# Optimization experiments

Measured on AMD Instinct MI355X. Metric: run time of the kernel, lower is better.

Reference implementation:

```python
import jax, jax.numpy as jnp
import numpy as np

H = 1024   # LSTM hidden (hardcoded in init_states)
A = 128    # attention / speaker dim
M = 80     # mel channels
TXT = 512  # text embedding dim
E = TXT + A
V = 185    # Flowtron symbol vocab
T = 512    # mel frames
TT = 192   # text tokens
SCALE = 0.05


def setup_inputs() -> dict:
    key = jax.random.key(0)
    ks = jax.random.split(key, 24)
    def rn(k, shape, s=SCALE):
        return jax.random.normal(k, shape, jnp.float32) * s
    return {
        "residual": jax.random.normal(ks[0], (1, M, T), jnp.float32),
        "speaker_vecs": jax.random.normal(ks[1], (1, A), jnp.float32),
        "emb": rn(ks[2], (V, TXT), 1.0),
        "Wih_att": rn(ks[3], (2, 4 * H, M)),
        "Whh_att": rn(ks[4], (2, 4 * H, H)),
        "b_att": jnp.zeros((2, 4 * H), jnp.float32),
        "Wq": rn(ks[5], (2, H, A)),
        "Wk": rn(ks[6], (2, E, A)),
        "Wv": rn(ks[7], (2, E, A)),
        "Wih1": rn(ks[8], (2, 4 * H, H + A)),
        "Whh1": rn(ks[9], (2, 4 * H, H)),
        "b1": jnp.zeros((2, 4 * H), jnp.float32),
        "Wih2": rn(ks[10], (2, 4 * H, H)),
        "Whh2": rn(ks[11], (2, 4 * H, H)),
        "b2": jnp.zeros((2, 4 * H), jnp.float32),
        "Wd": rn(ks[12], (2, H, H)),
        "bd": jnp.zeros((2, H), jnp.float32),
        "Wo": rn(ks[13], (2, H, 2 * M), 0.01),
        "bo": jnp.zeros((2, 2 * M), jnp.float32),
        "Wg": rn(ks[14], (2, H + A, 1)),
        "bg": jnp.zeros((2, 1), jnp.float32),
        "text": jax.random.randint(ks[15], (1, TT), 0, V),
    }


def _cell(x, h, c, Wih, Whh, b):
    # standard LSTM cell, gate order i,f,g,o
    z = x @ Wih.T + h @ Whh.T + b
    i, f, g, o = jnp.split(z, 4, axis=-1)
    c = jax.nn.sigmoid(f) * c + jax.nn.sigmoid(i) * jnp.tanh(g)
    h = jax.nn.sigmoid(o) * jnp.tanh(c)
    return h, c


def _run_flow(seq, enc, p, reverse):
    (Wih_att, Whh_att, b_att, Wq, Wk, Wv, Wih1, Whh1, b1,
     Wih2, Whh2, b2, Wd, bd, Wo, bo, Wg, bg) = p
    keys = enc @ Wk   # [TT, A] precomputed outside the scan
    vals = enc @ Wv   # [TT, A]
    inv = jnp.float32(1.0 / np.sqrt(A))
    def step(carry, x_t):
        prev, ha, ca, h1, c1, h2, c2 = carry
        ha, ca = _cell(prev, ha, ca, Wih_att, Whh_att, b_att)
        attn = jax.nn.softmax((ha @ Wq) @ keys.T * inv, axis=-1)  # [1, TT]
        ctx = attn @ vals                                          # [1, A]
        di = jnp.concatenate([ha, ctx], axis=-1)                   # [1, H+A]
        gate = jax.nn.sigmoid(di @ Wg + bg)  # gate computed; early-exit replaced by full-length scan
        h1, c1 = _cell(di, h1, c1, Wih1, Whh1, b1)
        h2, c2 = _cell(h1, h2, c2, Wih2, Whh2, b2)
        hd = jnp.tanh(h2 @ Wd + bd)
        out = hd @ Wo + bo
        b_p, log_s = jnp.split(out, 2, axis=-1)
        y = (x_t - b_p) * jnp.exp(-log_s)   # inverse affine coupling
        return (y, ha, ca, h1, c1, h2, c2), y
    z0 = jnp.zeros((1, M), seq.dtype)
    zh = jnp.zeros((1, H), seq.dtype)
    xs = seq[::-1] if reverse else seq
    _, ys = jax.lax.scan(step, (z0, zh, zh, zh, zh, zh, zh), xs)  # ys: [T, 1, M]
    return ys[::-1] if reverse else ys


def reference(residual, speaker_vecs, emb, Wih_att, Whh_att, b_att, Wq, Wk, Wv,
              Wih1, Whh1, b1, Wih2, Whh2, b2, Wd, bd, Wo, bo, Wg, bg, text):
    # encoder: text embedding concat broadcast speaker vector -> [TT, E]
    enc = jnp.concatenate(
        [emb[text[0]], jnp.broadcast_to(speaker_vecs, (text.shape[1], speaker_vecs.shape[1]))], axis=-1)
    stacked = (Wih_att, Whh_att, b_att, Wq, Wk, Wv, Wih1, Whh1, b1,
               Wih2, Whh2, b2, Wd, bd, Wo, bo, Wg, bg)
    seq = jnp.transpose(residual, (2, 0, 1))   # [T, 1, M]
    seq = _run_flow(seq, enc, tuple(w[1] for w in stacked), reverse=True)   # backward flow
    seq = _run_flow(seq, enc, tuple(w[0] for w in stacked), reverse=False)  # forward flow
    return jnp.transpose(seq, (1, 2, 0))       # [1, M, T]
```

## Files before the change

kernel.cpp:

```cpp
#include <hip/hip_runtime.h>
#include <hip/hip_bf16.h>
#include <stdint.h>

#define AG __HIP_MEMORY_SCOPE_AGENT
typedef unsigned long long ull;

static constexpr size_t OFF_WA  = 0;
static constexpr size_t OFF_W1  = 18874368;
static constexpr size_t OFF_W2  = 54657024;
static constexpr size_t OFF_WD  = 88342528;
static constexpr size_t OFF_WO  = 92536832;
static constexpr size_t OFF_WQ  = 93192192;
static constexpr size_t OFF_VL  = 93978624;
static constexpr size_t OFF_KEY = 94109696;
static constexpr size_t OFF_V32 = 94306304;
static constexpr size_t OFF_WQT = 94502912;
static constexpr size_t OFF_ENC = 95551488;
static constexpr size_t OFF_RB  = 96043008;
static constexpr size_t OFF_SEQ = 96206848;
static constexpr size_t OFF_DYN = 96370688;
static constexpr size_t OFF_HAb = OFF_DYN + 0;
static constexpr size_t OFF_H1b = OFF_DYN + 4096;
static constexpr size_t OFF_H2b = OFF_DYN + 8192;
static constexpr size_t OFF_HDb = OFF_DYN + 12288;
static constexpr size_t OFF_YBb = OFF_DYN + 16384;
static constexpr size_t OFF_SCb = OFF_DYN + 16896;
static constexpr size_t OFF_CXb = OFF_DYN + 17920;
static constexpr size_t OFF_FLG = OFF_DYN + 18432;
static constexpr size_t DYN_BYTES = 18432 + 229376;
static constexpr size_t NEEDED = OFF_DYN + DYN_BYTES;

#define PA 0
#define PS 1
#define P1 2
#define P2 3
#define PD 4
#define PF 5

__device__ __forceinline__ float aldx(const float* p){ return __hip_atomic_load(p, __ATOMIC_RELAXED, AG); }
__device__ __forceinline__ void  astx(float* p, float v){ __hip_atomic_store(p, v, __ATOMIC_RELAXED, AG); }
__device__ __forceinline__ ull   aldx8(const ull* p){ return __hip_atomic_load(p, __ATOMIC_RELAXED, AG); }
__device__ __forceinline__ int   ldi(const int* p){ return __hip_atomic_load(p, __ATOMIC_RELAXED, AG); }
__device__ __forceinline__ int   PADI(int k){ return k + ((k>>5)<<2); }

__device__ __forceinline__ float dot8(uint4 w, const float* v){
  float4 a = *(const float4*)v;
  float4 b = *(const float4*)(v+4);
  float s;
  s = __uint_as_float(w.x << 16) * a.x;
  s = fmaf(__uint_as_float(w.x & 0xffff0000u), a.y, s);
  s = fmaf(__uint_as_float(w.y << 16),         a.z, s);
  s = fmaf(__uint_as_float(w.y & 0xffff0000u), a.w, s);
  s = fmaf(__uint_as_float(w.z << 16),         b.x, s);
  s = fmaf(__uint_as_float(w.z & 0xffff0000u), b.y, s);
  s = fmaf(__uint_as_float(w.w << 16),         b.z, s);
  s = fmaf(__uint_as_float(w.w & 0xffff0000u), b.w, s);
  return s;
}
__device__ __forceinline__ float dot4(uint2 w, const float* v){
  float4 a = *(const float4*)v;
  float s;
  s = __uint_as_float(w.x << 16) * a.x;
  s = fmaf(__uint_as_float(w.x & 0xffff0000u), a.y, s);
  s = fmaf(__uint_as_float(w.y << 16),         a.z, s);
  s = fmaf(__uint_as_float(w.y & 0xffff0000u), a.w, s);
  return s;
}
__device__ __forceinline__ float sigf(float x){ return 1.f/(1.f+__expf(-x)); }
__device__ __forceinline__ float tanhf_(float x){
  x = fminf(12.f, fmaxf(-12.f, x));
  float t = __expf(2.f*x);
  return (t-1.f)/(t+1.f);
}

__global__ void k_init(float* z, int n){ int i = blockIdx.x*256 + threadIdx.x; if (i<n) z[i]=0.f; }

__global__ void k_rbuf(const float* res, float* rb){
  int i = blockIdx.x*256 + threadIdx.x; if (i >= 512*80) return;
  int t = i/80, m = i - t*80;
  rb[i] = res[m*512 + t];
}

__global__ void k_enc(const float* emb, const float* spk, const int* text, float* enc){
  int i = blockIdx.x*256 + threadIdx.x; if (i >= 192*640) return;
  int s = i/640, e = i - s*640;
  enc[i] = (e < 512) ? emb[(size_t)text[s]*512 + e] : spk[e-512];
}

__global__ void k_keysvals(const float* enc, const float* Wk, const float* Wv,
                           float* keys, float* vals32){
  int i = blockIdx.x*256 + threadIdx.x; if (i >= 2*192*128) return;
  int f = i/(192*128); int r = i - f*192*128; int s = r/128, a = r - s*128;
  float ka=0.f, va=0.f;
  for (int e=0;e<640;++e){
    float x = enc[s*640+e];
    ka = fmaf(x, Wk[((size_t)f*640+e)*128+a], ka);
    va = fmaf(x, Wv[((size_t)f*640+e)*128+a], va);
  }
  keys[((size_t)f*192+s)*128+a] = ka;
  vals32[((size_t)f*192+s)*128+a] = va;
}

__global__ void k_wqT(const float* Wq, float* WqT){
  int i = blockIdx.x*256 + threadIdx.x; if (i >= 2*128*1024) return;
  int f = i/(128*1024); int r = i - f*128*1024; int a = r/1024, h = r - a*1024;
  WqT[i] = Wq[((size_t)f*1024+h)*128+a];
}

__global__ void k_wqk2(const float* WqT, const float* keys, uint2* dst){
  int b = blockIdx.x; int f = b/192, s = b - f*192;
  int t = threadIdx.x;
  float4 acc = {0.f,0.f,0.f,0.f};
  const float* kp = keys + ((size_t)f*192+s)*128;
  const float* wp = WqT + (size_t)f*128*1024 + t*4;
  for (int a=0;a<128;++a){
    float kk = kp[a];
    float4 w = *(const float4*)(wp + (size_t)a*1024);
    acc.x = fmaf(kk, w.x, acc.x); acc.y = fmaf(kk, w.y, acc.y);
    acc.z = fmaf(kk, w.z, acc.z); acc.w = fmaf(kk, w.w, acc.w);
  }
  const float inv = 0.08838834764831845f;
  __hip_bfloat16 b0 = __float2bfloat16(acc.x*inv), b1 = __float2bfloat16(acc.y*inv);
  __hip_bfloat16 b2 = __float2bfloat16(acc.z*inv), b3 = __float2bfloat16(acc.w*inv);
  uint2 o;
  o.x = (uint32_t)(*(uint16_t*)&b0) | ((uint32_t)(*(uint16_t*)&b1) << 16);
  o.y = (uint32_t)(*(uint16_t*)&b2) | ((uint32_t)(*(uint16_t*)&b3) << 16);
  dst[((size_t)f*192+s)*256 + t] = o;
}

__device__ __forceinline__ uint32_t pk2(float a, float b){
  __hip_bfloat16 x = __float2bfloat16(a), y = __float2bfloat16(b);
  return (uint32_t)(*(uint16_t*)&x) | ((uint32_t)(*(uint16_t*)&y) << 16);
}

__global__ void k_packV2(const float* vals32, uint4* dst){
  int i = blockIdx.x*256 + threadIdx.x; if (i >= 2*192*16) return;
  int ag = i & 15; int r = i >> 4;
  int s = r % 192; int f = r / 192;
  float v[8];
  for (int e=0;e<8;++e) v[e] = vals32[((size_t)f*192+s)*128 + ag*8 + e];
  uint4 o; o.x = pk2(v[0],v[1]); o.y = pk2(v[2],v[3]); o.z = pk2(v[4],v[5]); o.w = pk2(v[6],v[7]);
  dst[i] = o;
}

__global__ void k_packA2(const float* Wih, const float* Whh, uint4* dst){
  int i = blockIdx.x*256 + threadIdx.x; if (i >= 2*256*256*9) return;
  int j = i % 9; int r = i / 9;
  int t = r & 255; r >>= 8;
  int b = r & 255; int f = r >> 8;
  int rs = t>>4, ks = t&15;
  int row = (rs>>2)*1024 + b*4 + (rs&3);
  float v[8];
  for (int e=0;e<8;++e){
    int c = ks*8 + e;
    if (j == 0) v[e] = (c < 80) ? Wih[((size_t)f*4096+row)*80 + c] : 0.f;
    else        v[e] = Whh[((size_t)f*4096+row)*1024 + (j-1)*128 + c];
  }
  uint4 o; o.x = pk2(v[0],v[1]); o.y = pk2(v[2],v[3]); o.z = pk2(v[4],v[5]); o.w = pk2(v[6],v[7]);
  dst[i] = o;
}

__global__ void k_pack1b(const float* Wih1, const float* Whh1, uint4* dst){
  int i = blockIdx.x*256 + threadIdx.x; if (i >= 2*256*16*273) return;
  int kc = i % 273; int r = i / 273;
  int rr = r & 15; r >>= 4;
  int b = r & 255; int f = r >> 8;
  int row = (rr>>2)*1024 + b*4 + (rr&3);
  int k0 = kc*8;
  float v[8];
  for (int e=0;e<8;++e){
    int k = k0+e; float x;
    if (k < 1024)      x = Wih1[((size_t)f*4096+row)*1152 + k];
    else if (k < 2048) x = Whh1[((size_t)f*4096+row)*1024 + (k-1024)];
    else if (k < 2176) x = Wih1[((size_t)f*4096+row)*1152 + 1024 + (k-2048)];
    else               x = 0.f;
    v[e] = x;
  }
  uint4 o; o.x = pk2(v[0],v[1]); o.y = pk2(v[2],v[3]); o.z = pk2(v[4],v[5]); o.w = pk2(v[6],v[7]);
  dst[i] = o;
}

__global__ void k_pack2b(const float* Wih2, const float* Whh2, uint4* dst){
  int i = blockIdx.x*256 + threadIdx.x; if (i >= 2*256*16*257) return;
  int kc = i % 257; int r = i / 257;
  int rr = r & 15; r >>= 4;
  int b = r & 255; int f = r >> 8;
  int row = (rr>>2)*1024 + b*4 + (rr&3);
  int k0 = kc*8;
  float v[8];
  for (int e=0;e<8;++e){
    int k = k0+e;
    v[e] = (k < 1024) ? Wih2[((size_t)f*4096+row)*1024 + k]
         : (k < 2048) ? Whh2[((size_t)f*4096+row)*1024 + (k-1024)] : 0.f;
  }
  uint4 o; o.x = pk2(v[0],v[1]); o.y = pk2(v[2],v[3]); o.z = pk2(v[4],v[5]); o.w = pk2(v[6],v[7]);
  dst[i] = o;
}

__global__ void k_packD2(const float* Wd, uint4* dst){
  __shared__ float tile[64][65];
  int b = blockIdx.x; int f = b >> 8; int rem = b & 255;
  int ot = rem >> 4, ct = rem & 15;
  int tid = threadIdx.x;
  for (int i = tid; i < 4096; i += 256){
    int rc = i >> 6, oc = i & 63;
    tile[rc][oc] = Wd[((size_t)f*1024 + ct*64 + rc)*1024 + ot*64 + oc];
  }
  __syncthreads();
  for (int w = 0; w < 2; ++w){
    int idx = w*256 + tid;
    int op = idx >> 3, cc = idx & 7;
    int k6 = (ct&7)*8 + cc, j = ct >> 3;
    int o = ot*64 + op;
    int b2 = o >> 2, r2 = o & 3;
    uint4 out;
    out.x = pk2(tile[cc*8+0][op], tile[cc*8+1][op]);
    out.y = pk2(tile[cc*8+2][op], tile[cc*8+3][op]);
    out.z = pk2(tile[cc*8+4][op], tile[cc*8+5][op]);
    out.w = pk2(tile[cc*8+6][op], tile[cc*8+7][op]);
    dst[((((size_t)f*256 + b2)*256) + r2*64 + k6)*2 + j] = out;
  }
}

__global__ void k_packO2(const float* Wo, uint2* dst){
  int i = blockIdx.x*256 + threadIdx.x; if (i >= 2*80*256) return;
  int t = i & 255; int r = i >> 8;
  int m = r % 80; int f = r / 80;
  for (int j = 0; j < 2; ++j){
    int row = m + j*80;
    float v[4];
    for (int e=0;e<4;++e) v[e] = Wo[((size_t)f*1024 + t*4+e)*160 + row];
    uint2 o; o.x = pk2(v[0],v[1]); o.y = pk2(v[2],v[3]);
    dst[(size_t)i*2 + j] = o;
  }
}

__launch_bounds__(256, 1)
__global__ void k_flow5(uint8_t* ws, int fl, int rev, int out_mode, int smode,
    const float* b_att_all, const float* b1_all, const float* b2_all,
    const float* bd_all, const float* bo_all,
    const float* xsrc, float* ydst)
{
  const int tid = threadIdx.x, bid = blockIdx.x;
  const int rs = tid >> 4, ks = tid & 15;
  const int wid = tid >> 6;
  const int ko = ks*8 + ((ks>>2)<<2);

  float* habuf = (float*)(ws + OFF_HAb);
  float* h1buf = (float*)(ws + OFF_H1b);
  float* h2buf = (float*)(ws + OFF_H2b);
  float* hdbuf = (float*)(ws + OFF_HDb);
  float* ybuf  = (float*)(ws + OFF_YBb);
  float* scb   = (float*)(ws + OFF_SCb);
  int*   flags = (int*)(ws + OFF_FLG);

  __shared__ __align__(16) ushort W1s[16*2184];
  __shared__ __align__(16) ushort W2s[16*2056];
  __shared__ __align__(16) float haPrevS[1152];
  __shared__ __align__(16) float S2[1152];
  __shared__ __align__(16) float S3[1152];
  __shared__ __align__(16) float scratch[2048];
  __shared__ __align__(16) float yS[144];
  __shared__ __align__(16) float ctxS[144];
  __shared__ __align__(16) float attp[288];
  __shared__ float zred[32];
  __shared__ float cst[3][4];
  __shared__ float bAs[16], b1s[16], b2s[16], bds[4], bos[2];

  const size_t fb = (size_t)fl*256 + bid;

  { const uint4* src = (const uint4*)((const ushort*)(ws + OFF_W1) + fb*16*2184);
    uint4* dst = (uint4*)W1s;
    for (int i = tid; i < 4368; i += 256) dst[i] = src[i]; }
  { const uint4* src = (const uint4*)((const ushort*)(ws + OFF_W2) + fb*16*2056);
    uint4* dst = (uint4*)W2s;
    for (int i = tid; i < 4112; i += 256) dst[i] = src[i]; }
  uint4 wa[9];
  { const uint4* g = (const uint4*)(ws + OFF_WA) + (fb*256 + tid)*9;
    #pragma unroll
    for (int j = 0; j < 9; ++j) wa[j] = g[j]; }
  uint4 wd[2];
  { const uint4* g = (const uint4*)(ws + OFF_WD) + (fb*256 + tid)*2;
    wd[0] = g[0]; wd[1] = g[1]; }
  uint2 wqk = {0,0};
  if (bid < 192) wqk = ((const uint2*)(ws + OFF_WQ))[((size_t)fl*192 + bid)*256 + tid];
  uint4 vals_r[12];
  { const uint4* g = (const uint4*)(ws + OFF_VL) + (((size_t)fl*192 + rs*12)*16 + ks);
    #pragma unroll
    for (int j = 0; j < 12; ++j) vals_r[j] = g[(size_t)j*16]; }
  uint2 wo0 = {0,0}, wo1 = {0,0};
  if (bid < 80){ const uint2* g = (const uint2*)(ws + OFF_WO) + (((size_t)fl*80 + bid)*256 + tid)*2;
    wo0 = g[0]; wo1 = g[1]; }
  if (tid < 16){
    int g = tid >> 2, uu = tid & 3;
    bAs[tid] = b_att_all[fl*4096 + g*1024 + bid*4 + uu];
    b1s[tid] = b1_all  [fl*4096 + g*1024 + bid*4 + uu];
    b2s[tid] = b2_all  [fl*4096 + g*1024 + bid*4 + uu];
  }
  if (tid < 4)  bds[tid] = bd_all[fl*1024 + bid*4 + tid];
  if (tid < 2 && bid < 80) bos[tid] = bo_all[fl*160 + tid*80 + bid];
  if (tid < 12) ((float*)cst)[tid] = 0.f;
  for (int i = tid; i < 1152; i += 256){ haPrevS[i]=0.f; S2[i]=0.f; S3[i]=0.f; }
  if (tid < 144){ yS[tid]=0.f; ctxS[tid]=0.f; }
  __syncthreads();

  auto SIG = [&](int ph, int tp1){
    __syncthreads();
    __builtin_amdgcn_sched_barrier(0);
    if (tid == 0){
      if (smode == 0) __hip_atomic_store(flags + (ph*256 + bid)*32, tp1, __ATOMIC_RELAXED, AG);
      else            __hip_atomic_fetch_add(flags + (ph*32 + (bid>>3))*32, 1, __ATOMIC_RELAXED, AG);
    }
  };
  auto WAITF = [&](int ph, int base, int n, int tp1){
    if (smode == 0){
      if (tid < n){
        const int* f = flags + (ph*256 + base + tid)*32;
        while (ldi(f) < tp1) __builtin_amdgcn_s_sleep(1);
      }
    } else {
      int nl = n >> 3, bl = base >> 3, tgt = tp1*8;
      if (tid < nl){
        const int* f = flags + (ph*32 + bl + tid)*32;
        while (ldi(f) < tgt) __builtin_amdgcn_s_sleep(1);
      }
    }
    __syncthreads();
  };
  auto stage_pad = [&](const float* g, float* s){
    const ull* g8 = (const ull*)g;
    #pragma unroll
    for (int i = tid; i < 512; i += 256){
      ull v = aldx8(g8 + i);
      int k = i*2;
      *(ull*)&s[k + ((k>>5)<<2)] = v;
    }
  };

  const uint4* w1row = (const uint4*)(W1s) + (size_t)rs*273;
  const uint4* w2row = (const uint4*)(W2s) + (size_t)rs*257;

  float accA = 0.f;

  for (int t = 0; t < 512; ++t) {
    const int col = rev ? (511 - t) : t;
    const int tp1 = t + 1;
    float x = 0.f;
    if (bid < 80) x = xsrc[col*80 + bid];

    {
      float acc = accA + dot8(wa[0], yS + ko);
      acc += __shfl_xor(acc,1); acc += __shfl_xor(acc,2);
      acc += __shfl_xor(acc,4); acc += __shfl_xor(acc,8);
      if (ks == 0) zred[rs] = acc + bAs[rs];
    }
    __syncthreads();
    if (tid < 4) {
      float zi=zred[tid], zf=zred[4+tid], zg=zred[8+tid], zo=zred[12+tid];
      float c = sigf(zf)*cst[0][tid] + sigf(zi)*tanhf_(zg);
      float h = sigf(zo)*tanhf_(c);
      cst[0][tid] = c;
      astx(habuf + bid*4 + tid, h);
    }
    SIG(PA, tp1);

    float acc1 = 0.f, acc2 = 0.f;
    #pragma unroll
    for (int j = 0; j < 8; ++j) acc1 += dot8(w1row[(j+8)*16 + ks], S2 + j*144 + ko);
    #pragma unroll
    for (int j = 0; j < 8; ++j) acc2 += dot8(w2row[(j+8)*16 + ks], S3 + j*144 + ko);

    WAITF(PA, 0, 256, tp1);
    stage_pad(habuf, haPrevS);
    __syncthreads();

    if (bid < 192) {
      float sv = dot4(wqk, haPrevS + tid*4 + ((tid>>3)<<2));
      #pragma unroll
      for (int d=1; d<64; d<<=1) sv += __shfl_xor(sv, d);
      if ((tid&63) == 0) zred[16+wid] = sv;
      __syncthreads();
      if (tid == 0) astx(scb + bid, zred[16]+zred[17]+zred[18]+zred[19]);
      SIG(PS, tp1);
    }

    #pragma unroll
    for (int j = 0; j < 8; ++j) acc1 += dot8(w1row[j*16 + ks], haPrevS + j*144 + ko);

    WAITF(PS, 0, 192, tp1);
    if (tid < 96){ ull v = aldx8((const ull*)scb + tid); int k=tid*2;
                   *(ull*)&attp[k + ((k>>5)<<2)] = v; }
    __syncthreads();
    {
      float v = (tid < 192) ? attp[PADI(tid)] : -3.0e38f;
      float m = v;
      #pragma unroll
      for (int d=1; d<64; d<<=1) m = fmaxf(m, __shfl_xor(m, d));
      if ((tid&63) == 0) zred[16+wid] = m;
      __syncthreads();
      float mx = fmaxf(fmaxf(zred[16],zred[17]), fmaxf(zred[18],zred[19]));
      float e = (tid < 192) ? __expf(v - mx) : 0.f;
      float sm = e;
      #pragma unroll
      for (int d=1; d<64; d<<=1) sm += __shfl_xor(sm, d);
      if ((tid&63) == 0) zred[20+wid] = sm;
      __syncthreads();
      float inv = 1.f / (zred[20]+zred[21]+zred[22]+zred[23]);
      attp[PADI(tid)] = (tid < 192) ? e * inv : 0.f;
    }
    __syncthreads();
    {
      float pc0=0,pc1=0,pc2=0,pc3=0,pc4=0,pc5=0,pc6=0,pc7=0;
      #pragma unroll
      for (int j = 0; j < 12; ++j){
        float pj = attp[PADI(rs*12 + j)];
        uint4 v = vals_r[j];
        pc0 = fmaf(__uint_as_float(v.x << 16),         pj, pc0);
        pc1 = fmaf(__uint_as_float(v.x & 0xffff0000u), pj, pc1);
        pc2 = fmaf(__uint_as_float(v.y << 16),         pj, pc2);
        pc3 = fmaf(__uint_as_float(v.y & 0xffff0000u), pj, pc3);
        pc4 = fmaf(__uint_as_float(v.z << 16),         pj, pc4);
        pc5 = fmaf(__uint_as_float(v.z & 0xffff0000u), pj, pc5);
        pc6 = fmaf(__uint_as_float(v.w << 16),         pj, pc6);
        pc7 = fmaf(__uint_as_float(v.w & 0xffff0000u), pj, pc7);
      }
      *(float4*)&scratch[tid*8]   = make_float4(pc0,pc1,pc2,pc3);
      *(float4*)&scratch[tid*8+4] = make_float4(pc4,pc5,pc6,pc7);
    }
    __syncthreads();
    if (tid < 128){
      float s = 0.f;
      #pragma unroll
      for (int sg = 0; sg < 16; ++sg) s += scratch[sg*128 + tid];
      ctxS[PADI(tid)] = s;
    }
    __syncthreads();

    {
      acc1 += dot8(w1row[256 + ks], ctxS + ko);
      acc1 += __shfl_xor(acc1,1); acc1 += __shfl_xor(acc1,2);
      acc1 += __shfl_xor(acc1,4); acc1 += __shfl_xor(acc1,8);
      if (ks == 0) zred[rs] = acc1 + b1s[rs];
    }
    __syncthreads();
    if (tid < 4) {
      float zi=zred[tid], zf=zred[4+tid], zg=zred[8+tid], zo=zred[12+tid];
      float c = sigf(zf)*cst[1][tid] + sigf(zi)*tanhf_(zg);
      float h = sigf(zo)*tanhf_(c);
      cst[1][tid] = c;
      astx(h1buf + bid*4 + tid, h);
    }
    SIG(P1, tp1);

    {
      float a = 0.f;
      #pragma unroll
      for (int j = 1; j < 9; ++j) a += dot8(wa[j], haPrevS + (j-1)*144 + ko);
      accA = a;
    }

    WAITF(P1, 0, 256, tp1);
    stage_pad(h1buf, S2);
    __syncthreads();

    {
      #pragma unroll
      for (int j = 0; j < 8; ++j) acc2 += dot8(w2row[j*16 + ks], S2 + j*144 + ko);
      acc2 += __shfl_xor(acc2,1); acc2 += __shfl_xor(acc2,2);
      acc2 += __shfl_xor(acc2,4); acc2 += __shfl_xor(acc2,8);
      if (ks == 0) zred[rs] = acc2 + b2s[rs];
    }
    __syncthreads();
    if (tid < 4) {
      float zi=zred[tid], zf=zred[4+tid], zg=zred[8+tid], zo=zred[12+tid];
      float c = sigf(zf)*cst[2][tid] + sigf(zi)*tanhf_(zg);
      float h = sigf(zo)*tanhf_(c);
      cst[2][tid] = c;
      astx(h2buf + bid*4 + tid, h);
    }
    SIG(P2, tp1);
    WAITF(P2, 0, 256, tp1);
    stage_pad(h2buf, S3);
    __syncthreads();

    {
      int k6 = tid & 63, r2 = tid >> 6;
      int kk = k6*8 + ((k6>>2)<<2);
      float acc = dot8(wd[0], S3 + kk) + dot8(wd[1], S3 + 576 + kk);
      #pragma unroll
      for (int d=1; d<64; d<<=1) acc += __shfl_xor(acc, d);
      if (k6 == 0) astx(hdbuf + bid*4 + r2, tanhf_(acc + bds[r2]));
    }
    SIG(PD, tp1);

    if (bid < 80) {
      WAITF(PD, 0, 256, tp1);
      stage_pad(hdbuf, scratch);
      __syncthreads();
      int po = tid*4 + ((tid>>3)<<2);
      float pb = dot4(wo0, scratch + po);
      float pl = dot4(wo1, scratch + po);
      #pragma unroll
      for (int d=1; d<64; d<<=1) { pb += __shfl_xor(pb, d); pl += __shfl_xor(pl, d); }
      if ((tid & 63) == 0) { zred[16+wid] = pb; zred[20+wid] = pl; }
      __syncthreads();
      if (tid == 0) {
        float bp = zred[16]+zred[17]+zred[18]+zred[19] + bos[0];
        float ls = zred[20]+zred[21]+zred[22]+zred[23] + bos[1];
        float y = (x - bp) * __expf(-ls);
        if (out_mode == 0) ydst[col*80 + bid] = y;
        else               ydst[bid*512 + col] = y;
        astx(ybuf + bid, y);
      }
      SIG(PF, tp1);
    }
    WAITF(PF, 0, 80, tp1);
    if (tid < 64){ ull v = (tid < 40) ? aldx8((const ull*)ybuf + tid) : 0ull;
                   int k = tid*2; *(ull*)&yS[k + ((k>>5)<<2)] = v; }
    __syncthreads();
  }
}

extern "C" void kernel_launch(void* const* d_in, const int* in_sizes, int n_in,
                              void* d_out, int out_size, void* d_ws, size_t ws_size,
                              hipStream_t stream) {
  if (ws_size < NEEDED) return;
  uint8_t* ws = (uint8_t*)d_ws;
  const float* residual = (const float*)d_in[0];
  const float* spk      = (const float*)d_in[1];
  const float* emb      = (const float*)d_in[2];
  const float* Wih_att  = (const float*)d_in[3];
  const float* Whh_att  = (const float*)d_in[4];
  const float* b_att    = (const float*)d_in[5];
  const float* Wq       = (const float*)d_in[6];
  const float* Wk       = (const float*)d_in[7];
  const float* Wv       = (const float*)d_in[8];
  const float* Wih1     = (const float*)d_in[9];
  const float* Whh1     = (const float*)d_in[10];
  const float* b1       = (const float*)d_in[11];
  const float* Wih2     = (const float*)d_in[12];
  const float* Whh2     = (const float*)d_in[13];
  const float* b2       = (const float*)d_in[14];
  const float* Wd       = (const float*)d_in[15];
  const float* bd       = (const float*)d_in[16];
  const float* Wo       = (const float*)d_in[17];
  const float* bo       = (const float*)d_in[18];
  const int*   text     = (const int*)d_in[21];

  dim3 B(256);
  k_rbuf<<<160, B, 0, stream>>>(residual, (float*)(ws+OFF_RB));
  k_enc<<<480, B, 0, stream>>>(emb, spk, text, (float*)(ws+OFF_ENC));
  k_keysvals<<<192, B, 0, stream>>>((const float*)(ws+OFF_ENC), Wk, Wv,
                                    (float*)(ws+OFF_KEY), (float*)(ws+OFF_V32));
  k_wqT<<<1024, B, 0, stream>>>(Wq, (float*)(ws+OFF_WQT));
  k_wqk2<<<384, B, 0, stream>>>((const float*)(ws+OFF_WQT), (const float*)(ws+OFF_KEY),
                                (uint2*)(ws+OFF_WQ));
  k_packV2<<<24, B, 0, stream>>>((const float*)(ws+OFF_V32), (uint4*)(ws+OFF_VL));
  k_packA2<<<4608, B, 0, stream>>>(Wih_att, Whh_att, (uint4*)(ws+OFF_WA));
  k_pack1b<<<8736, B, 0, stream>>>(Wih1, Whh1, (uint4*)(ws+OFF_W1));
  k_pack2b<<<8224, B, 0, stream>>>(Wih2, Whh2, (uint4*)(ws+OFF_W2));
  k_packD2<<<512, B, 0, stream>>>(Wd, (uint4*)(ws+OFF_WD));
  k_packO2<<<160, B, 0, stream>>>(Wo, (uint2*)(ws+OFF_WO));

  k_init<<<242, B, 0, stream>>>((float*)(ws+OFF_DYN), (int)(DYN_BYTES/4));
  k_flow5<<<256, B, 0, stream>>>(ws, 1, 1, 0, 0, b_att, b1, b2, bd, bo,
                                 (const float*)(ws+OFF_RB), (float*)(ws+OFF_SEQ));
  k_init<<<242, B, 0, stream>>>((float*)(ws+OFF_DYN), (int)(DYN_BYTES/4));
  k_flow5<<<256, B, 0, stream>>>(ws, 0, 0, 1, 1, b_att, b1, b2, bd, bo,
                                 (const float*)(ws+OFF_SEQ), (float*)d_out);
}
```

Baseline: 23.39 ms.

## Replace per-phase flag barriers with tagged-data polling on payload values

Drops the separate flag arrays and signal/wait barriers between persistent blocks. Each published value instead carries a 2-bit step tag in its low mantissa bits, and consumers spin on the data itself until every element shows the current tag. This removes the flag round trip and a __syncthreads per phase, which should shorten the per-timestep critical path of the recurrent chain. In exchange it loses the two low mantissa bits of each exchanged value, and every thread polls up to four global words instead of a few threads polling flags.

```diff
diff --git a/kernel.cpp b/kernel.cpp
--- a/kernel.cpp
+++ b/kernel.cpp
@@ -25,23 +25,15 @@
 static constexpr size_t OFF_HDb = OFF_DYN + 12288;
 static constexpr size_t OFF_YBb = OFF_DYN + 16384;
 static constexpr size_t OFF_SCb = OFF_DYN + 16896;
-static constexpr size_t OFF_CXb = OFF_DYN + 17920;
-static constexpr size_t OFF_FLG = OFF_DYN + 18432;
-static constexpr size_t DYN_BYTES = 18432 + 229376;
+static constexpr size_t DYN_BYTES = 18432;
 static constexpr size_t NEEDED = OFF_DYN + DYN_BYTES;
-
-#define PA 0
-#define PS 1
-#define P1 2
-#define P2 3
-#define PD 4
-#define PF 5
 
 __device__ __forceinline__ float aldx(const float* p){ return __hip_atomic_load(p, __ATOMIC_RELAXED, AG); }
 __device__ __forceinline__ void  astx(float* p, float v){ __hip_atomic_store(p, v, __ATOMIC_RELAXED, AG); }
-__device__ __forceinline__ ull   aldx8(const ull* p){ return __hip_atomic_load(p, __ATOMIC_RELAXED, AG); }
-__device__ __forceinline__ int   ldi(const int* p){ return __hip_atomic_load(p, __ATOMIC_RELAXED, AG); }
 __device__ __forceinline__ int   PADI(int k){ return k + ((k>>5)<<2); }
+__device__ __forceinline__ float tagf(float f, uint32_t tag){
+  return __uint_as_float((__float_as_uint(f) & ~3u) | tag);
+}
 
 __device__ __forceinline__ float dot8(uint4 w, const float* v){
   float4 a = *(const float4*)v;
@@ -236,7 +228,7 @@
 }
 
 __launch_bounds__(256, 1)
-__global__ void k_flow5(uint8_t* ws, int fl, int rev, int out_mode, int smode,
+__global__ void k_flow6(uint8_t* ws, int fl, int rev, int out_mode,
     const float* b_att_all, const float* b1_all, const float* b2_all,
     const float* bd_all, const float* bo_all,
     const float* xsrc, float* ydst)
@@ -252,7 +244,6 @@
   float* hdbuf = (float*)(ws + OFF_HDb);
   float* ybuf  = (float*)(ws + OFF_YBb);
   float* scb   = (float*)(ws + OFF_SCb);
-  int*   flags = (int*)(ws + OFF_FLG);
 
   __shared__ __align__(16) ushort W1s[16*2184];
   __shared__ __align__(16) ushort W2s[16*2056];
@@ -304,36 +295,26 @@
   if (tid < 144){ yS[tid]=0.f; ctxS[tid]=0.f; }
   __syncthreads();
 
-  auto SIG = [&](int ph, int tp1){
-    __syncthreads();
-    __builtin_amdgcn_sched_barrier(0);
-    if (tid == 0){
-      if (smode == 0) __hip_atomic_store(flags + (ph*256 + bid)*32, tp1, __ATOMIC_RELAXED, AG);
-      else            __hip_atomic_fetch_add(flags + (ph*32 + (bid>>3))*32, 1, __ATOMIC_RELAXED, AG);
-    }
+  auto poll4 = [&](const float* g, float* s, uint32_t tag){
+    float v0,v1,v2,v3;
+    bool o0=false,o1=false,o2=false,o3=false;
+    for(;;){
+      if(!o0){ float f=aldx(g+tid);     if((__float_as_uint(f)&3u)==tag){v0=f;o0=true;} }
+      if(!o1){ float f=aldx(g+tid+256); if((__float_as_uint(f)&3u)==tag){v1=f;o1=true;} }
+      if(!o2){ float f=aldx(g+tid+512); if((__float_as_uint(f)&3u)==tag){v2=f;o2=true;} }
+      if(!o3){ float f=aldx(g+tid+768); if((__float_as_uint(f)&3u)==tag){v3=f;o3=true;} }
+      if(o0&&o1&&o2&&o3) break;
+      __builtin_amdgcn_s_sleep(1);
+    }
+    s[PADI(tid)]     = v0;  s[PADI(tid+256)] = v1;
+    s[PADI(tid+512)] = v2;  s[PADI(tid+768)] = v3;
   };
-  auto WAITF = [&](int ph, int base, int n, int tp1){
-    if (smode == 0){
-      if (tid < n){
-        const int* f = flags + (ph*256 + base + tid)*32;
-        while (ldi(f) < tp1) __builtin_amdgcn_s_sleep(1);
-      }
-    } else {
-      int nl = n >> 3, bl = base >> 3, tgt = tp1*8;
-      if (tid < nl){
-        const int* f = flags + (ph*32 + bl + tid)*32;
-        while (ldi(f) < tgt) __builtin_amdgcn_s_sleep(1);
-      }
-    }
-    __syncthreads();
-  };
-  auto stage_pad = [&](const float* g, float* s){
-    const ull* g8 = (const ull*)g;
-    #pragma unroll
-    for (int i = tid; i < 512; i += 256){
-      ull v = aldx8(g8 + i);
-      int k = i*2;
-      *(ull*)&s[k + ((k>>5)<<2)] = v;
+  auto poll1 = [&](const float* g, int n, float* s, uint32_t tag){
+    if (tid < n){
+      float f;
+      for(;;){ f = aldx(g+tid); if((__float_as_uint(f)&3u)==tag) break;
+               __builtin_amdgcn_s_sleep(1); }
+      s[PADI(tid)] = f;
     }
   };
 
@@ -344,7 +325,7 @@
 
   for (int t = 0; t < 512; ++t) {
     const int col = rev ? (511 - t) : t;
-    const int tp1 = t + 1;
+    const uint32_t TAG = (uint32_t)((t+1) & 3);
     float x = 0.f;
     if (bid < 80) x = xsrc[col*80 + bid];
 
@@ -360,9 +341,8 @@
       float c = sigf(zf)*cst[0][tid] + sigf(zi)*tanhf_(zg);
       float h = sigf(zo)*tanhf_(c);
       cst[0][tid] = c;
-      astx(habuf + bid*4 + tid, h);
-    }
-    SIG(PA, tp1);
+      astx(habuf + bid*4 + tid, tagf(h, TAG));
+    }
 
     float acc1 = 0.f, acc2 = 0.f;
     #pragma unroll
@@ -370,8 +350,7 @@
     #pragma unroll
     for (int j = 0; j < 8; ++j) acc2 += dot8(w2row[(j+8)*16 + ks], S3 + j*144 + ko);
 
-    WAITF(PA, 0, 256, tp1);
-    stage_pad(habuf, haPrevS);
+    poll4(habuf, haPrevS, TAG);
     __syncthreads();
 
     if (bid < 192) {
@@ -380,17 +359,15 @@
       for (int d=1; d<64; d<<=1) sv += __shfl_xor(sv, d);
       if ((tid&63) == 0) zred[16+wid] = sv;
       __syncthreads();
-      if (tid == 0) astx(scb + bid, zred[16]+zred[17]+zred[18]+zred[19]);
-      SIG(PS, tp1);
+      if (tid == 0) astx(scb + bid, tagf(zred[16]+zred[17]+zred[18]+zred[19], TAG));
     }
 
     #pragma unroll
     for (int j = 0; j < 8; ++j) acc1 += dot8(w1row[j*16 + ks], haPrevS + j*144 + ko);
 
-    WAITF(PS, 0, 192, tp1);
-    if (tid < 96){ ull v = aldx8((const ull*)scb + tid); int k=tid*2;
-                   *(ull*)&attp[k + ((k>>5)<<2)] = v; }
-    __syncthreads();
+    poll1(scb, 192, attp, TAG);
+    __syncthreads();
+
     {
       float v = (tid < 192) ? attp[PADI(tid)] : -3.0e38f;
       float m = v;
@@ -448,9 +425,8 @@
       float c = sigf(zf)*cst[1][tid] + sigf(zi)*tanhf_(zg);
       float h = sigf(zo)*tanhf_(c);
       cst[1][tid] = c;
-      astx(h1buf + bid*4 + tid, h);
-    }
-    SIG(P1, tp1);
+      astx(h1buf + bid*4 + tid, tagf(h, TAG));
+    }
 
     {
       float a = 0.f;
@@ -459,8 +435,7 @@
       accA = a;
     }
 
-    WAITF(P1, 0, 256, tp1);
-    stage_pad(h1buf, S2);
+    poll4(h1buf, S2, TAG);
     __syncthreads();
 
     {
@@ -476,11 +451,10 @@
       float c = sigf(zf)*cst[2][tid] + sigf(zi)*tanhf_(zg);
       float h = sigf(zo)*tanhf_(c);
       cst[2][tid] = c;
-      astx(h2buf + bid*4 + tid, h);
-    }
-    SIG(P2, tp1);
-    WAITF(P2, 0, 256, tp1);
-    stage_pad(h2buf, S3);
+      astx(h2buf + bid*4 + tid, tagf(h, TAG));
+    }
+
+    poll4(h2buf, S3, TAG);
     __syncthreads();
 
     {
@@ -489,13 +463,11 @@
       float acc = dot8(wd[0], S3 + kk) + dot8(wd[1], S3 + 576 + kk);
       #pragma unroll
       for (int d=1; d<64; d<<=1) acc += __shfl_xor(acc, d);
-      if (k6 == 0) astx(hdbuf + bid*4 + r2, tanhf_(acc + bds[r2]));
-    }
-    SIG(PD, tp1);
+      if (k6 == 0) astx(hdbuf + bid*4 + r2, tagf(tanhf_(acc + bds[r2]), TAG));
+    }
 
     if (bid < 80) {
-      WAITF(PD, 0, 256, tp1);
-      stage_pad(hdbuf, scratch);
+      poll4(hdbuf, scratch, TAG);
       __syncthreads();
       int po = tid*4 + ((tid>>3)<<2);
       float pb = dot4(wo0, scratch + po);
@@ -510,13 +482,11 @@
         float y = (x - bp) * __expf(-ls);
         if (out_mode == 0) ydst[col*80 + bid] = y;
         else               ydst[bid*512 + col] = y;
-        astx(ybuf + bid, y);
+        astx(ybuf + bid, tagf(y, TAG));
       }
-      SIG(PF, tp1);
-    }
-    WAITF(PF, 0, 80, tp1);
-    if (tid < 64){ ull v = (tid < 40) ? aldx8((const ull*)ybuf + tid) : 0ull;
-                   int k = tid*2; *(ull*)&yS[k + ((k>>5)<<2)] = v; }
+    }
+
+    poll1(ybuf, 80, yS, TAG);
     __syncthreads();
   }
 }
@@ -562,10 +532,10 @@
   k_packD2<<<512, B, 0, stream>>>(Wd, (uint4*)(ws+OFF_WD));
   k_packO2<<<160, B, 0, stream>>>(Wo, (uint2*)(ws+OFF_WO));
 
-  k_init<<<242, B, 0, stream>>>((float*)(ws+OFF_DYN), (int)(DYN_BYTES/4));
-  k_flow5<<<256, B, 0, stream>>>(ws, 1, 1, 0, 0, b_att, b1, b2, bd, bo,
+  k_init<<<18, B, 0, stream>>>((float*)(ws+OFF_DYN), (int)(DYN_BYTES/4));
+  k_flow6<<<256, B, 0, stream>>>(ws, 1, 1, 0, b_att, b1, b2, bd, bo,
                                  (const float*)(ws+OFF_RB), (float*)(ws+OFF_SEQ));
-  k_init<<<242, B, 0, stream>>>((float*)(ws+OFF_DYN), (int)(DYN_BYTES/4));
-  k_flow5<<<256, B, 0, stream>>>(ws, 0, 0, 1, 1, b_att, b1, b2, bd, bo,
+  k_init<<<18, B, 0, stream>>>((float*)(ws+OFF_DYN), (int)(DYN_BYTES/4));
+  k_flow6<<<256, B, 0, stream>>>(ws, 0, 0, 1, b_att, b1, b2, bd, bo,
                                  (const float*)(ws+OFF_SEQ), (float*)d_out);
 }
```

Measured after the change: 24.96 ms. +6.7%, slower.
